# Kernel optimization log

Measured on AMD Instinct MI355X. Metric: run time of the kernel, lower is better.

## Reference

```python
import jax, jax.numpy as jnp
import numpy as np

N_NODES = 1048576
N_SEG = 16384
NODES_PER_SEG = N_NODES // N_SEG
D = 128
EPS = 1e-5


def setup_inputs() -> dict:
    key = jax.random.key(0)
    ks = jax.random.split(key, 8)
    feat = jax.random.normal(ks[0], (N_NODES, D), dtype=jnp.float32)
    position_weight = jax.random.uniform(ks[1], (N_NODES,), dtype=jnp.float32)
    # equal-size segments (sessions): contiguous, sorted segment ids
    segment_ids = jnp.repeat(jnp.arange(N_SEG, dtype=jnp.int32), NODES_PER_SEG)
    # last node of each segment
    last_nodes = jnp.arange(N_SEG, dtype=jnp.int32) * NODES_PER_SEG + (NODES_PER_SEG - 1)
    # parameters
    gamma = jnp.ones((D,), dtype=jnp.float32)
    beta = jnp.zeros((D,), dtype=jnp.float32)
    s = 1.0 / np.sqrt(D)
    W_u = jax.random.uniform(ks[2], (D, D), dtype=jnp.float32, minval=-s, maxval=s)
    W_i = jax.random.uniform(ks[3], (D, D), dtype=jnp.float32, minval=-s, maxval=s)
    b_i = jax.random.uniform(ks[4], (D,), dtype=jnp.float32, minval=-s, maxval=s)
    w_e = jax.random.uniform(ks[5], (D,), dtype=jnp.float32, minval=-s, maxval=s)
    return {
        "feat": feat, "position_weight": position_weight,
        "last_nodes": last_nodes, "segment_ids": segment_ids,
        "gamma": gamma, "beta": beta, "W_u": W_u, "W_i": W_i,
        "b_i": b_i, "w_e": w_e, "num_segments": N_SEG,
    }


def reference(feat, position_weight, last_nodes, segment_ids, gamma, beta,
              W_u, W_i, b_i, w_e, num_segments):
    # BatchNorm1d (training-mode batch statistics)
    mean = feat.mean(axis=0)
    var = jnp.mean((feat - mean) ** 2, axis=0)
    f = (feat - mean) * (gamma / jnp.sqrt(var + EPS)) + beta  # [N, D]

    feat_u = f @ W_u.T                                         # [N, H]
    feat_last = f[last_nodes] @ W_i.T + b_i                    # [B, H]
    # broadcast_nodes: gather per-graph vector back to its nodes
    e = jax.nn.sigmoid(feat_u + feat_last[segment_ids]) @ w_e  # [N]

    # segment softmax over nodes of each graph
    m = jax.ops.segment_max(e, segment_ids, num_segments=num_segments)
    ex = jnp.exp(e - m[segment_ids])
    denom = jax.ops.segment_sum(ex, segment_ids, num_segments=num_segments)
    alpha = ex / denom[segment_ids]                            # [N]

    rst = jax.ops.segment_sum(f * alpha[:, None], segment_ids,
                              num_segments=num_segments)       # [B, D]
    position_rst = jax.ops.segment_sum(f * position_weight[:, None], segment_ids,
                                       num_segments=num_segments)  # [B, D]
    return rst, position_rst
```

## Files before the change

### kernel.cpp

```cpp
#include <hip/hip_runtime.h>

#define N_NODES 1048576
#define N_SEG   16384
#define NPS     64
#define D       128
#define EPS     1e-5f

typedef float f4 __attribute__((ext_vector_type(4)));
typedef float f32x4 __attribute__((ext_vector_type(4)));
typedef __bf16 bf16x8 __attribute__((ext_vector_type(8)));

__global__ __launch_bounds__(256) void k_stats(const float* __restrict__ feat,
                                               float* __restrict__ part) {
    int t = threadIdx.x;
    long gid = (long)blockIdx.x * 256 + t;
    const f4* f4p = (const f4*)feat;
    f4 s = {0.f,0.f,0.f,0.f}, q = {0.f,0.f,0.f,0.f};
#pragma unroll 8
    for (int k = 0; k < 64; ++k) {
        f4 v = f4p[gid + (long)k * 524288];
        s += v;
        q += v * v;
    }
    __shared__ f4 red[2][8][32];
    red[0][t >> 5][t & 31] = s;
    red[1][t >> 5][t & 31] = q;
    __syncthreads();
    int stat = t >> 7, c = t & 127;
    const float* base = (const float*)&red[stat][0][0];
    float acc = 0.f;
#pragma unroll
    for (int r = 0; r < 8; ++r) acc += base[r * 128 + c];
    part[(stat * 128 + c) * 2048 + blockIdx.x] = acc;
}

__global__ __launch_bounds__(256) void k_scale(const float* __restrict__ part,
                                               const float* __restrict__ gamma,
                                               const float* __restrict__ beta,
                                               float* __restrict__ scl,
                                               float* __restrict__ shf) {
    int t = threadIdx.x, c = blockIdx.x;
    float s1 = 0.f, s2 = 0.f;
#pragma unroll
    for (int j = 0; j < 8; ++j) {
        s1 += part[c * 2048 + t + 256 * j];
        s2 += part[(128 + c) * 2048 + t + 256 * j];
    }
    __shared__ float rs[256], rq[256];
    rs[t] = s1; rq[t] = s2;
    __syncthreads();
    for (int off = 128; off > 0; off >>= 1) {
        if (t < off) { rs[t] += rs[t + off]; rq[t] += rq[t + off]; }
        __syncthreads();
    }
    if (t == 0) {
        float mean = rs[0] / (float)N_NODES;
        float var  = rq[0] / (float)N_NODES - mean * mean;
        float sc   = gamma[c] * rsqrtf(var + EPS);
        scl[c] = sc;
        shf[c] = beta[c] - mean * sc;
    }
}

__device__ inline unsigned pk2(float x, float y) {
    unsigned a = __builtin_bit_cast(unsigned, x);
    unsigned b = __builtin_bit_cast(unsigned, y);
    a = (a + 0x7fffu + ((a >> 16) & 1u)) >> 16;
    b = (b + 0x7fffu + ((b >> 16) & 1u)) & 0xffff0000u;
    return a | b;
}
__device__ inline bf16x8 lds8(const unsigned short* p, int row, int kb) {
    int addr = (row * 256 + kb) ^ ((row & 7) << 4);
    return *(const bf16x8*)((const char*)p + addr);
}

__global__ __launch_bounds__(256)
void k_main(const float* __restrict__ feat,
            const float* __restrict__ pw,
            const float* __restrict__ Wu,
            const float* __restrict__ Wi,
            const float* __restrict__ bi,
            const float* __restrict__ we,
            const float* __restrict__ scl,
            const float* __restrict__ shf,
            float* __restrict__ out) {
    __shared__ __align__(16) unsigned short sW[128 * 128];
    __shared__ __align__(16) unsigned short abuf[64 * 128];
    __shared__ float flp_s[8][128];
    __shared__ float pw_s[512];
    __shared__ float epart[4][64];
    __shared__ float wpR[4][128];
    __shared__ float wpP[4][128];

    int t = threadIdx.x;
    int lane = t & 63, w = t >> 6;
    int l15 = lane & 15, g4 = lane >> 4;
    int c0 = 4 * (t & 31);
    f4 vscl = *(const f4*)(scl + c0);
    f4 vshf = *(const f4*)(shf + c0);
    int h_a = l15 + 32 * w;
    int h_b = h_a + 16;
    int seg0 = blockIdx.x * 8;

    pw_s[t] = pw[seg0 * NPS + t];
    pw_s[t + 256] = pw[seg0 * NPS + t + 256];
    {
        int r = t >> 5;
        long row = (long)(seg0 + r) * NPS + (NPS - 1);
        f4 v = *(const f4*)(feat + row * 128 + c0);
        v = v * vscl + vshf;
        int addr = (r * 256 + 8 * (t & 31)) ^ ((r & 7) << 4);
        *(uint2*)((char*)abuf + addr) = make_uint2(pk2(v.x, v.y), pk2(v.z, v.w));
        int r2 = r + 8;
        int addr2 = (r2 * 256 + 8 * (t & 31)) ^ ((r2 & 7) << 4);
        *(uint2*)((char*)abuf + addr2) = make_uint2(0u, 0u);
    }
    {
        const f4* W4 = (const f4*)Wi;
#pragma unroll
        for (int k = 0; k < 16; ++k) {
            int g = t + 256 * k, h = g >> 5, cq = g & 31;
            f4 v = W4[g];
            int addr = (h * 256 + cq * 8) ^ ((h & 7) << 4);
            *(uint2*)((char*)sW + addr) = make_uint2(pk2(v.x, v.y), pk2(v.z, v.w));
        }
    }
    __syncthreads();
    {
        f32x4 a2[2];
        a2[0] = (f32x4){0.f,0.f,0.f,0.f};
        a2[1] = (f32x4){0.f,0.f,0.f,0.f};
#pragma unroll
        for (int kk = 0; kk < 4; ++kk) {
            int kb = kk * 64 + g4 * 16;
            bf16x8 a = lds8(abuf, l15, kb);
            a2[0] = __builtin_amdgcn_mfma_f32_16x16x32_bf16(a, lds8(sW, h_a, kb), a2[0], 0, 0, 0);
            a2[1] = __builtin_amdgcn_mfma_f32_16x16x32_bf16(a, lds8(sW, h_b, kb), a2[1], 0, 0, 0);
        }
        float bia = bi[h_a], bib = bi[h_b];
#pragma unroll
        for (int r = 0; r < 4; ++r) {
            int si = 4 * g4 + r;
            if (si < 8) {
                flp_s[si][h_a] = a2[0][r] + bia;
                flp_s[si][h_b] = a2[1][r] + bib;
            }
        }
    }
    __syncthreads();
    {
        const f4* W4 = (const f4*)Wu;
#pragma unroll
        for (int k = 0; k < 16; ++k) {
            int g = t + 256 * k, h = g >> 5, cq = g & 31;
            f4 v = W4[g];
            int addr = (h * 256 + cq * 8) ^ ((h & 7) << 4);
            *(uint2*)((char*)sW + addr) = make_uint2(pk2(v.x, v.y), pk2(v.z, v.w));
        }
    }
    float we0 = we[h_a], we1 = we[h_b];
    __syncthreads();

    for (int it = 0; it < 8; ++it) {
        int seg = seg0 + it;
        {
            const f4* src = (const f4*)(feat + (long)seg * NPS * D);
#pragma unroll
            for (int k = 0; k < 8; ++k) {
                f4 v = src[t + 256 * k] * vscl + vshf;
                int n = (t >> 5) + 8 * k;
                int addr = (n * 256 + 8 * (t & 31)) ^ ((n & 7) << 4);
                *(uint2*)((char*)abuf + addr) = make_uint2(pk2(v.x, v.y), pk2(v.z, v.w));
            }
        }
        __syncthreads();

        float fl0 = flp_s[it][h_a];
        float fl1 = flp_s[it][h_b];
        float eacc[4][4];
#pragma unroll
        for (int nf = 0; nf < 4; ++nf)
#pragma unroll
            for (int r = 0; r < 4; ++r) eacc[nf][r] = 0.f;
#pragma unroll
        for (int hfp = 0; hfp < 2; ++hfp) {
            int h = hfp ? h_b : h_a;
            float flh = hfp ? fl1 : fl0;
            float weh = hfp ? we1 : we0;
            f32x4 acc[4];
#pragma unroll
            for (int nf = 0; nf < 4; ++nf) acc[nf] = (f32x4){0.f,0.f,0.f,0.f};
#pragma unroll
            for (int kk = 0; kk < 4; ++kk) {
                int kb = kk * 64 + g4 * 16;
                bf16x8 b = lds8(sW, h, kb);
#pragma unroll
                for (int nf = 0; nf < 4; ++nf) {
                    bf16x8 a = lds8(abuf, l15 + 16 * nf, kb);
                    acc[nf] = __builtin_amdgcn_mfma_f32_16x16x32_bf16(a, b, acc[nf], 0, 0, 0);
                }
            }
#pragma unroll
            for (int nf = 0; nf < 4; ++nf)
#pragma unroll
                for (int r = 0; r < 4; ++r) {
                    float x = acc[nf][r] + flh;
                    eacc[nf][r] += weh * __frcp_rn(1.f + __expf(-x));
                }
        }
#pragma unroll
        for (int nf = 0; nf < 4; ++nf) {
#pragma unroll
            for (int r = 0; r < 4; ++r) {
                float p = eacc[nf][r];
                p += __shfl_xor(p, 1);
                p += __shfl_xor(p, 2);
                p += __shfl_xor(p, 4);
                p += __shfl_xor(p, 8);
                if (l15 == 0) epart[w][16 * nf + 4 * g4 + r] = p;
            }
        }
        __syncthreads();

        float e = epart[0][lane] + epart[1][lane] + epart[2][lane] + epart[3][lane];
        float m = e;
#pragma unroll
        for (int off = 32; off > 0; off >>= 1) m = fmaxf(m, __shfl_xor(m, off));
        float ex = __expf(e - m);
        float sd = ex;
#pragma unroll
        for (int off = 32; off > 0; off >>= 1) sd += __shfl_xor(sd, off);
        float al = ex / sd;

        f4 racc = {0.f,0.f,0.f,0.f}, pacc = {0.f,0.f,0.f,0.f};
#pragma unroll
        for (int k = 0; k < 8; ++k) {
            int n = (t >> 5) + 8 * k;
            int addr = (n * 256 + 8 * (t & 31)) ^ ((n & 7) << 4);
            uint2 u = *(const uint2*)((const char*)abuf + addr);
            f4 fv;
            fv.x = __builtin_bit_cast(float, u.x << 16);
            fv.y = __builtin_bit_cast(float, u.x & 0xffff0000u);
            fv.z = __builtin_bit_cast(float, u.y << 16);
            fv.w = __builtin_bit_cast(float, u.y & 0xffff0000u);
            float av = __shfl(al, n);
            float pv = pw_s[it * NPS + n];
            racc += av * fv;
            pacc += pv * fv;
        }
#pragma unroll
        for (int c = 0; c < 4; ++c) {
            racc[c] += __shfl_xor(racc[c], 32);
            pacc[c] += __shfl_xor(pacc[c], 32);
        }
        if (lane < 32) {
            *(f4*)&wpR[w][4 * lane] = racc;
            *(f4*)&wpP[w][4 * lane] = pacc;
        }
        __syncthreads();

        if (t < 128) {
            out[(long)seg * 128 + t] = wpR[0][t] + wpR[1][t] + wpR[2][t] + wpR[3][t];
        } else {
            int c = t - 128;
            out[(long)N_SEG * 128 + (long)seg * 128 + c] =
                wpP[0][c] + wpP[1][c] + wpP[2][c] + wpP[3][c];
        }
    }
}

extern "C" void kernel_launch(void* const* d_in, const int* in_sizes, int n_in,
                              void* d_out, int out_size, void* d_ws, size_t ws_size,
                              hipStream_t stream) {
    const float* feat       = (const float*)d_in[0];
    const float* pw         = (const float*)d_in[1];
    const float* gamma      = (const float*)d_in[4];
    const float* beta       = (const float*)d_in[5];
    const float* Wu         = (const float*)d_in[6];
    const float* Wi         = (const float*)d_in[7];
    const float* bi         = (const float*)d_in[8];
    const float* we         = (const float*)d_in[9];
    float* out = (float*)d_out;

    float* ws   = (float*)d_ws;
    float* part = ws;
    float* wscl = ws + 524288;
    float* wshf = ws + 524288 + 128;

    k_stats<<<dim3(2048), dim3(256), 0, stream>>>(feat, part);
    k_scale<<<dim3(128),  dim3(256), 0, stream>>>(part, gamma, beta, wscl, wshf);
    k_main <<<dim3(2048), dim3(256), 0, stream>>>(feat, pw, Wu, Wi, bi, we, wscl, wshf, out);
}
```

Before: 358.5 us.

## Assign whole segments per wavefront, loading MFMA operands directly from global memory

```diff
diff --git a/kernel.cpp b/kernel.cpp
--- a/kernel.cpp
+++ b/kernel.cpp
@@ -85,35 +85,31 @@
             const float* __restrict__ shf,
             float* __restrict__ out) {
     __shared__ __align__(16) unsigned short sW[128 * 128];
-    __shared__ __align__(16) unsigned short abuf[64 * 128];
+    __shared__ __align__(16) unsigned short sA8[16 * 128];
     __shared__ float flp_s[8][128];
-    __shared__ float pw_s[512];
-    __shared__ float epart[4][64];
-    __shared__ float wpR[4][128];
-    __shared__ float wpP[4][128];
+    __shared__ float scl_s[128], shf_s[128], we_s[128];
+    __shared__ float alpha_w[4][64];
+    __shared__ float pw_w[4][64];
 
     int t = threadIdx.x;
     int lane = t & 63, w = t >> 6;
     int l15 = lane & 15, g4 = lane >> 4;
     int c0 = 4 * (t & 31);
-    f4 vscl = *(const f4*)(scl + c0);
-    f4 vshf = *(const f4*)(shf + c0);
-    int h_a = l15 + 32 * w;
-    int h_b = h_a + 16;
     int seg0 = blockIdx.x * 8;
 
-    pw_s[t] = pw[seg0 * NPS + t];
-    pw_s[t + 256] = pw[seg0 * NPS + t + 256];
+    if (t < 128) { scl_s[t] = scl[t]; shf_s[t] = shf[t]; we_s[t] = we[t]; }
     {
         int r = t >> 5;
         long row = (long)(seg0 + r) * NPS + (NPS - 1);
         f4 v = *(const f4*)(feat + row * 128 + c0);
-        v = v * vscl + vshf;
+        f4 vs = *(const f4*)(scl + c0);
+        f4 vh = *(const f4*)(shf + c0);
+        v = v * vs + vh;
         int addr = (r * 256 + 8 * (t & 31)) ^ ((r & 7) << 4);
-        *(uint2*)((char*)abuf + addr) = make_uint2(pk2(v.x, v.y), pk2(v.z, v.w));
+        *(uint2*)((char*)sA8 + addr) = make_uint2(pk2(v.x, v.y), pk2(v.z, v.w));
         int r2 = r + 8;
         int addr2 = (r2 * 256 + 8 * (t & 31)) ^ ((r2 & 7) << 4);
-        *(uint2*)((char*)abuf + addr2) = make_uint2(0u, 0u);
+        *(uint2*)((char*)sA8 + addr2) = make_uint2(0u, 0u);
     }
     {
         const f4* W4 = (const f4*)Wi;
@@ -127,13 +123,14 @@
     }
     __syncthreads();
     {
+        int h_a = l15 + 32 * w, h_b = h_a + 16;
         f32x4 a2[2];
         a2[0] = (f32x4){0.f,0.f,0.f,0.f};
         a2[1] = (f32x4){0.f,0.f,0.f,0.f};
 #pragma unroll
         for (int kk = 0; kk < 4; ++kk) {
             int kb = kk * 64 + g4 * 16;
-            bf16x8 a = lds8(abuf, l15, kb);
+            bf16x8 a = lds8(sA8, l15, kb);
             a2[0] = __builtin_amdgcn_mfma_f32_16x16x32_bf16(a, lds8(sW, h_a, kb), a2[0], 0, 0, 0);
             a2[1] = __builtin_amdgcn_mfma_f32_16x16x32_bf16(a, lds8(sW, h_b, kb), a2[1], 0, 0, 0);
         }
@@ -158,113 +155,95 @@
             *(uint2*)((char*)sW + addr) = make_uint2(pk2(v.x, v.y), pk2(v.z, v.w));
         }
     }
-    float we0 = we[h_a], we1 = we[h_b];
-    __syncthreads();
-
-    for (int it = 0; it < 8; ++it) {
-        int seg = seg0 + it;
-        {
-            const f4* src = (const f4*)(feat + (long)seg * NPS * D);
-#pragma unroll
-            for (int k = 0; k < 8; ++k) {
-                f4 v = src[t + 256 * k] * vscl + vshf;
-                int n = (t >> 5) + 8 * k;
-                int addr = (n * 256 + 8 * (t & 31)) ^ ((n & 7) << 4);
-                *(uint2*)((char*)abuf + addr) = make_uint2(pk2(v.x, v.y), pk2(v.z, v.w));
+    __syncthreads();
+
+    for (int s = 0; s < 2; ++s) {
+        int sl = 2 * w + s, seg = seg0 + sl;
+        const float* fb = feat + (long)seg * NPS * D;
+
+        pw_w[w][lane] = pw[seg * NPS + lane];
+
+        float e_c[4];
+#pragma unroll
+        for (int c = 0; c < 4; ++c) {
+            bf16x8 af[4];
+#pragma unroll
+            for (int kk = 0; kk < 4; ++kk) {
+                int d0 = kk * 32 + g4 * 8;
+                const float* p = fb + (16 * c + l15) * 128 + d0;
+                f4 u = *(const f4*)p, v = *(const f4*)(p + 4);
+                f4 s1 = *(const f4*)&scl_s[d0], s2 = *(const f4*)&scl_s[d0 + 4];
+                f4 h1 = *(const f4*)&shf_s[d0], h2 = *(const f4*)&shf_s[d0 + 4];
+                u = u * s1 + h1;
+                v = v * s2 + h2;
+                unsigned r0 = pk2(u.x, u.y), r1 = pk2(u.z, u.w);
+                unsigned r2 = pk2(v.x, v.y), r3 = pk2(v.z, v.w);
+                uint4 rr = make_uint4(r0, r1, r2, r3);
+                af[kk] = __builtin_bit_cast(bf16x8, rr);
             }
-        }
-        __syncthreads();
-
-        float fl0 = flp_s[it][h_a];
-        float fl1 = flp_s[it][h_b];
-        float eacc[4][4];
-#pragma unroll
-        for (int nf = 0; nf < 4; ++nf)
-#pragma unroll
-            for (int r = 0; r < 4; ++r) eacc[nf][r] = 0.f;
-#pragma unroll
-        for (int hfp = 0; hfp < 2; ++hfp) {
-            int h = hfp ? h_b : h_a;
-            float flh = hfp ? fl1 : fl0;
-            float weh = hfp ? we1 : we0;
-            f32x4 acc[4];
-#pragma unroll
-            for (int nf = 0; nf < 4; ++nf) acc[nf] = (f32x4){0.f,0.f,0.f,0.f};
-#pragma unroll
-            for (int kk = 0; kk < 4; ++kk) {
-                int kb = kk * 64 + g4 * 16;
-                bf16x8 b = lds8(sW, h, kb);
-#pragma unroll
-                for (int nf = 0; nf < 4; ++nf) {
-                    bf16x8 a = lds8(abuf, l15 + 16 * nf, kb);
-                    acc[nf] = __builtin_amdgcn_mfma_f32_16x16x32_bf16(a, b, acc[nf], 0, 0, 0);
+            float eacc = 0.f;
+#pragma unroll
+            for (int hf = 0; hf < 8; ++hf) {
+                f32x4 acc = (f32x4){0.f,0.f,0.f,0.f};
+#pragma unroll
+                for (int kk = 0; kk < 4; ++kk) {
+                    bf16x8 wuf = lds8(sW, 16 * hf + l15, kk * 64 + g4 * 16);
+                    acc = __builtin_amdgcn_mfma_f32_16x16x32_bf16(wuf, af[kk], acc, 0, 0, 0);
+                }
+                f4 flp4 = *(const f4*)&flp_s[sl][16 * hf + 4 * g4];
+                f4 we4  = *(const f4*)&we_s[16 * hf + 4 * g4];
+#pragma unroll
+                for (int r = 0; r < 4; ++r) {
+                    float x = acc[r] + flp4[r];
+                    eacc += we4[r] * __frcp_rn(1.f + __expf(-x));
                 }
             }
-#pragma unroll
-            for (int nf = 0; nf < 4; ++nf)
-#pragma unroll
-                for (int r = 0; r < 4; ++r) {
-                    float x = acc[nf][r] + flh;
-                    eacc[nf][r] += weh * __frcp_rn(1.f + __expf(-x));
-                }
-        }
-#pragma unroll
-        for (int nf = 0; nf < 4; ++nf) {
-#pragma unroll
-            for (int r = 0; r < 4; ++r) {
-                float p = eacc[nf][r];
-                p += __shfl_xor(p, 1);
-                p += __shfl_xor(p, 2);
-                p += __shfl_xor(p, 4);
-                p += __shfl_xor(p, 8);
-                if (l15 == 0) epart[w][16 * nf + 4 * g4 + r] = p;
-            }
-        }
-        __syncthreads();
-
-        float e = epart[0][lane] + epart[1][lane] + epart[2][lane] + epart[3][lane];
-        float m = e;
-#pragma unroll
-        for (int off = 32; off > 0; off >>= 1) m = fmaxf(m, __shfl_xor(m, off));
-        float ex = __expf(e - m);
-        float sd = ex;
-#pragma unroll
-        for (int off = 32; off > 0; off >>= 1) sd += __shfl_xor(sd, off);
-        float al = ex / sd;
-
+            eacc += __shfl_xor(eacc, 16);
+            eacc += __shfl_xor(eacc, 32);
+            e_c[c] = eacc;
+        }
+
+        float m = fmaxf(fmaxf(e_c[0], e_c[1]), fmaxf(e_c[2], e_c[3]));
+#pragma unroll
+        for (int off = 8; off > 0; off >>= 1) m = fmaxf(m, __shfl_xor(m, off));
+        float a0 = __expf(e_c[0] - m), a1 = __expf(e_c[1] - m);
+        float a2 = __expf(e_c[2] - m), a3 = __expf(e_c[3] - m);
+        float sd = a0 + a1 + a2 + a3;
+#pragma unroll
+        for (int off = 8; off > 0; off >>= 1) sd += __shfl_xor(sd, off);
+        float inv = 1.f / sd;
+        if (g4 == 0) {
+            alpha_w[w][l15]      = a0 * inv;
+            alpha_w[w][16 + l15] = a1 * inv;
+            alpha_w[w][32 + l15] = a2 * inv;
+            alpha_w[w][48 + l15] = a3 * inv;
+        }
+        float spw = pw_w[w][lane];
+#pragma unroll
+        for (int off = 32; off > 0; off >>= 1) spw += __shfl_xor(spw, off);
+
+        int q = lane >> 5, cc = lane & 31;
         f4 racc = {0.f,0.f,0.f,0.f}, pacc = {0.f,0.f,0.f,0.f};
-#pragma unroll
-        for (int k = 0; k < 8; ++k) {
-            int n = (t >> 5) + 8 * k;
-            int addr = (n * 256 + 8 * (t & 31)) ^ ((n & 7) << 4);
-            uint2 u = *(const uint2*)((const char*)abuf + addr);
-            f4 fv;
-            fv.x = __builtin_bit_cast(float, u.x << 16);
-            fv.y = __builtin_bit_cast(float, u.x & 0xffff0000u);
-            fv.z = __builtin_bit_cast(float, u.y << 16);
-            fv.w = __builtin_bit_cast(float, u.y & 0xffff0000u);
-            float av = __shfl(al, n);
-            float pv = pw_s[it * NPS + n];
-            racc += av * fv;
-            pacc += pv * fv;
-        }
-#pragma unroll
-        for (int c = 0; c < 4; ++c) {
-            racc[c] += __shfl_xor(racc[c], 32);
-            pacc[c] += __shfl_xor(pacc[c], 32);
+#pragma unroll 4
+        for (int k = 0; k < 32; ++k) {
+            int n = q + 2 * k;
+            f4 v = *(const f4*)(fb + n * 128 + cc * 4);
+            float al = alpha_w[w][n];
+            float pv = pw_w[w][n];
+            racc += al * v;
+            pacc += pv * v;
+        }
+#pragma unroll
+        for (int j = 0; j < 4; ++j) {
+            racc[j] += __shfl_xor(racc[j], 32);
+            pacc[j] += __shfl_xor(pacc[j], 32);
         }
         if (lane < 32) {
-            *(f4*)&wpR[w][4 * lane] = racc;
-            *(f4*)&wpP[w][4 * lane] = pacc;
-        }
-        __syncthreads();
-
-        if (t < 128) {
-            out[(long)seg * 128 + t] = wpR[0][t] + wpR[1][t] + wpR[2][t] + wpR[3][t];
-        } else {
-            int c = t - 128;
-            out[(long)N_SEG * 128 + (long)seg * 128 + c] =
-                wpP[0][c] + wpP[1][c] + wpP[2][c] + wpP[3][c];
+            f4 sc4 = *(const f4*)&scl_s[4 * cc];
+            f4 sh4 = *(const f4*)&shf_s[4 * cc];
+            *(f4*)(out + (long)seg * 128 + 4 * cc) = sc4 * racc + sh4;
+            *(f4*)(out + (long)N_SEG * 128 + (long)seg * 128 + 4 * cc) =
+                sc4 * pacc + sh4 * spw;
         }
     }
 }
```

Result: slower. 517.8 us (+44.4%).

## Process two segments per iteration and prefetch next pair's features into registers

Applied to the files above, without the earlier changes.

```diff
diff --git a/kernel.cpp b/kernel.cpp
--- a/kernel.cpp
+++ b/kernel.cpp
@@ -73,6 +73,12 @@
     int addr = (row * 256 + kb) ^ ((row & 7) << 4);
     return *(const bf16x8*)((const char*)p + addr);
 }
+__device__ inline void barx() {
+    __builtin_amdgcn_sched_barrier(0);
+    asm volatile("s_waitcnt lgkmcnt(0)");
+    __builtin_amdgcn_s_barrier();
+    __builtin_amdgcn_sched_barrier(0);
+}
 
 __global__ __launch_bounds__(256)
 void k_main(const float* __restrict__ feat,
@@ -85,12 +91,11 @@
             const float* __restrict__ shf,
             float* __restrict__ out) {
     __shared__ __align__(16) unsigned short sW[128 * 128];
-    __shared__ __align__(16) unsigned short abuf[64 * 128];
+    __shared__ __align__(16) unsigned short abuf[128 * 128];
     __shared__ float flp_s[8][128];
-    __shared__ float pw_s[512];
-    __shared__ float epart[4][64];
-    __shared__ float wpR[4][128];
-    __shared__ float wpP[4][128];
+    __shared__ float epart[4][128];
+    __shared__ float wpR[2][4][128];
+    __shared__ float wpP[2][4][128];
 
     int t = threadIdx.x;
     int lane = t & 63, w = t >> 6;
@@ -98,12 +103,17 @@
     int c0 = 4 * (t & 31);
     f4 vscl = *(const f4*)(scl + c0);
     f4 vshf = *(const f4*)(shf + c0);
-    int h_a = l15 + 32 * w;
-    int h_b = h_a + 16;
+    int h_a = l15 + 32 * w, h_b = h_a + 16;
     int seg0 = blockIdx.x * 8;
 
-    pw_s[t] = pw[seg0 * NPS + t];
-    pw_s[t + 256] = pw[seg0 * NPS + t + 256];
+    f4 fn[16];
+    {
+        const f4* src = (const f4*)(feat + (long)seg0 * NPS * D);
+#pragma unroll
+        for (int k = 0; k < 16; ++k) fn[k] = src[t + 256 * k];
+    }
+    __builtin_amdgcn_sched_barrier(0);
+
     {
         int r = t >> 5;
         long row = (long)(seg0 + r) * NPS + (NPS - 1);
@@ -125,7 +135,7 @@
             *(uint2*)((char*)sW + addr) = make_uint2(pk2(v.x, v.y), pk2(v.z, v.w));
         }
     }
-    __syncthreads();
+    barx();
     {
         f32x4 a2[2];
         a2[0] = (f32x4){0.f,0.f,0.f,0.f};
@@ -147,7 +157,7 @@
             }
         }
     }
-    __syncthreads();
+    barx();
     {
         const f4* W4 = (const f4*)Wu;
 #pragma unroll
@@ -159,82 +169,93 @@
         }
     }
     float we0 = we[h_a], we1 = we[h_b];
-    __syncthreads();
-
-    for (int it = 0; it < 8; ++it) {
-        int seg = seg0 + it;
-        {
-            const f4* src = (const f4*)(feat + (long)seg * NPS * D);
-#pragma unroll
-            for (int k = 0; k < 8; ++k) {
-                f4 v = src[t + 256 * k] * vscl + vshf;
-                int n = (t >> 5) + 8 * k;
-                int addr = (n * 256 + 8 * (t & 31)) ^ ((n & 7) << 4);
-                *(uint2*)((char*)abuf + addr) = make_uint2(pk2(v.x, v.y), pk2(v.z, v.w));
-            }
-        }
-        __syncthreads();
-
-        float fl0 = flp_s[it][h_a];
-        float fl1 = flp_s[it][h_b];
-        float eacc[4][4];
-#pragma unroll
-        for (int nf = 0; nf < 4; ++nf)
-#pragma unroll
-            for (int r = 0; r < 4; ++r) eacc[nf][r] = 0.f;
-#pragma unroll
-        for (int hfp = 0; hfp < 2; ++hfp) {
-            int h = hfp ? h_b : h_a;
-            float flh = hfp ? fl1 : fl0;
-            float weh = hfp ? we1 : we0;
-            f32x4 acc[4];
-#pragma unroll
-            for (int nf = 0; nf < 4; ++nf) acc[nf] = (f32x4){0.f,0.f,0.f,0.f};
-#pragma unroll
-            for (int kk = 0; kk < 4; ++kk) {
-                int kb = kk * 64 + g4 * 16;
-                bf16x8 b = lds8(sW, h, kb);
-#pragma unroll
-                for (int nf = 0; nf < 4; ++nf) {
-                    bf16x8 a = lds8(abuf, l15 + 16 * nf, kb);
-                    acc[nf] = __builtin_amdgcn_mfma_f32_16x16x32_bf16(a, b, acc[nf], 0, 0, 0);
-                }
-            }
-#pragma unroll
-            for (int nf = 0; nf < 4; ++nf)
-#pragma unroll
-                for (int r = 0; r < 4; ++r) {
-                    float x = acc[nf][r] + flh;
-                    eacc[nf][r] += weh * __frcp_rn(1.f + __expf(-x));
-                }
-        }
-#pragma unroll
-        for (int nf = 0; nf < 4; ++nf) {
-#pragma unroll
-            for (int r = 0; r < 4; ++r) {
-                float p = eacc[nf][r];
-                p += __shfl_xor(p, 1);
-                p += __shfl_xor(p, 2);
-                p += __shfl_xor(p, 4);
-                p += __shfl_xor(p, 8);
-                if (l15 == 0) epart[w][16 * nf + 4 * g4 + r] = p;
-            }
-        }
-        __syncthreads();
-
-        float e = epart[0][lane] + epart[1][lane] + epart[2][lane] + epart[3][lane];
-        float m = e;
-#pragma unroll
-        for (int off = 32; off > 0; off >>= 1) m = fmaxf(m, __shfl_xor(m, off));
-        float ex = __expf(e - m);
-        float sd = ex;
-#pragma unroll
-        for (int off = 32; off > 0; off >>= 1) sd += __shfl_xor(sd, off);
-        float al = ex / sd;
-
-        f4 racc = {0.f,0.f,0.f,0.f}, pacc = {0.f,0.f,0.f,0.f};
-#pragma unroll
-        for (int k = 0; k < 8; ++k) {
+    barx();
+
+#define GATE_SEG(SL, RB)                                                          \
+    do {                                                                          \
+        float fl0_ = flp_s[(SL)][h_a];                                            \
+        float fl1_ = flp_s[(SL)][h_b];                                            \
+        f32x4 acc[4][2];                                                          \
+        _Pragma("unroll")                                                         \
+        for (int nf = 0; nf < 4; ++nf) {                                          \
+            acc[nf][0] = (f32x4){0.f,0.f,0.f,0.f};                                \
+            acc[nf][1] = (f32x4){0.f,0.f,0.f,0.f};                                \
+        }                                                                         \
+        _Pragma("unroll")                                                         \
+        for (int kk = 0; kk < 4; ++kk) {                                          \
+            int kb = kk * 64 + g4 * 16;                                           \
+            bf16x8 a[4];                                                          \
+            _Pragma("unroll")                                                     \
+            for (int nf = 0; nf < 4; ++nf) a[nf] = lds8(abuf, (RB) + l15 + 16 * nf, kb); \
+            _Pragma("unroll")                                                     \
+            for (int nf = 0; nf < 4; ++nf) {                                      \
+                acc[nf][0] = __builtin_amdgcn_mfma_f32_16x16x32_bf16(a[nf], lds8(sW, h_a, kb), acc[nf][0], 0, 0, 0); \
+                acc[nf][1] = __builtin_amdgcn_mfma_f32_16x16x32_bf16(a[nf], lds8(sW, h_b, kb), acc[nf][1], 0, 0, 0); \
+            }                                                                     \
+        }                                                                         \
+        _Pragma("unroll")                                                         \
+        for (int nf = 0; nf < 4; ++nf) {                                          \
+            _Pragma("unroll")                                                     \
+            for (int r = 0; r < 4; ++r) {                                         \
+                float x0 = acc[nf][0][r] + fl0_;                                  \
+                float x1 = acc[nf][1][r] + fl1_;                                  \
+                float p = we0 * __frcp_rn(1.f + __expf(-x0))                      \
+                        + we1 * __frcp_rn(1.f + __expf(-x1));                     \
+                p += __shfl_xor(p, 1);                                            \
+                p += __shfl_xor(p, 2);                                            \
+                p += __shfl_xor(p, 4);                                            \
+                p += __shfl_xor(p, 8);                                            \
+                if (l15 == 0) epart[w][(RB) + 16 * nf + 4 * g4 + r] = p;          \
+            }                                                                     \
+        }                                                                         \
+    } while (0)
+
+    for (int it = 0; it < 4; ++it) {
+        int sA = 2 * it, sB = 2 * it + 1;
+        int segA = seg0 + sA, segB = seg0 + sB;
+
+#pragma unroll
+        for (int k = 0; k < 16; ++k) {
+            f4 v = fn[k] * vscl + vshf;
+            int n = (t >> 5) + 8 * k;
+            int addr = (n * 256 + 8 * (t & 31)) ^ ((n & 7) << 4);
+            *(uint2*)((char*)abuf + addr) = make_uint2(pk2(v.x, v.y), pk2(v.z, v.w));
+        }
+        barx();
+        if (it < 3) {
+            const f4* src = (const f4*)(feat + (long)(seg0 + 2 * it + 2) * NPS * D);
+#pragma unroll
+            for (int k = 0; k < 16; ++k) fn[k] = src[t + 256 * k];
+        }
+        __builtin_amdgcn_sched_barrier(0);
+
+        GATE_SEG(sA, 0);
+        GATE_SEG(sB, 64);
+        barx();
+
+        float eA = epart[0][lane] + epart[1][lane] + epart[2][lane] + epart[3][lane];
+        float eB = epart[0][64 + lane] + epart[1][64 + lane]
+                 + epart[2][64 + lane] + epart[3][64 + lane];
+        float mA = eA, mB = eB;
+#pragma unroll
+        for (int off = 32; off > 0; off >>= 1) {
+            mA = fmaxf(mA, __shfl_xor(mA, off));
+            mB = fmaxf(mB, __shfl_xor(mB, off));
+        }
+        float exA = __expf(eA - mA), exB = __expf(eB - mB);
+        float sdA = exA, sdB = exB;
+#pragma unroll
+        for (int off = 32; off > 0; off >>= 1) {
+            sdA += __shfl_xor(sdA, off);
+            sdB += __shfl_xor(sdB, off);
+        }
+        float alA = exA / sdA;
+        float alB = exB / sdB;
+
+        f4 rA = {0.f,0.f,0.f,0.f}, pA = {0.f,0.f,0.f,0.f};
+        f4 rB = {0.f,0.f,0.f,0.f}, pB = {0.f,0.f,0.f,0.f};
+#pragma unroll
+        for (int k = 0; k < 16; ++k) {
             int n = (t >> 5) + 8 * k;
             int addr = (n * 256 + 8 * (t & 31)) ^ ((n & 7) << 4);
             uint2 u = *(const uint2*)((const char*)abuf + addr);
@@ -243,30 +264,48 @@
             fv.y = __builtin_bit_cast(float, u.x & 0xffff0000u);
             fv.z = __builtin_bit_cast(float, u.y << 16);
             fv.w = __builtin_bit_cast(float, u.y & 0xffff0000u);
-            float av = __shfl(al, n);
-            float pv = pw_s[it * NPS + n];
-            racc += av * fv;
-            pacc += pv * fv;
+            if (k < 8) {
+                float av = __shfl(alA, n);
+                float pv = pw[segA * NPS + n];
+                rA += av * fv;
+                pA += pv * fv;
+            } else {
+                int nb = n - 64;
+                float av = __shfl(alB, nb);
+                float pv = pw[segB * NPS + nb];
+                rB += av * fv;
+                pB += pv * fv;
+            }
         }
 #pragma unroll
         for (int c = 0; c < 4; ++c) {
-            racc[c] += __shfl_xor(racc[c], 32);
-            pacc[c] += __shfl_xor(pacc[c], 32);
+            rA[c] += __shfl_xor(rA[c], 32);
+            pA[c] += __shfl_xor(pA[c], 32);
+            rB[c] += __shfl_xor(rB[c], 32);
+            pB[c] += __shfl_xor(pB[c], 32);
         }
         if (lane < 32) {
-            *(f4*)&wpR[w][4 * lane] = racc;
-            *(f4*)&wpP[w][4 * lane] = pacc;
-        }
-        __syncthreads();
+            *(f4*)&wpR[0][w][4 * lane] = rA;
+            *(f4*)&wpP[0][w][4 * lane] = pA;
+            *(f4*)&wpR[1][w][4 * lane] = rB;
+            *(f4*)&wpP[1][w][4 * lane] = pB;
+        }
+        barx();
 
         if (t < 128) {
-            out[(long)seg * 128 + t] = wpR[0][t] + wpR[1][t] + wpR[2][t] + wpR[3][t];
+            out[(long)segA * 128 + t] =
+                wpR[0][0][t] + wpR[0][1][t] + wpR[0][2][t] + wpR[0][3][t];
+            out[(long)segB * 128 + t] =
+                wpR[1][0][t] + wpR[1][1][t] + wpR[1][2][t] + wpR[1][3][t];
         } else {
             int c = t - 128;
-            out[(long)N_SEG * 128 + (long)seg * 128 + c] =
-                wpP[0][c] + wpP[1][c] + wpP[2][c] + wpP[3][c];
-        }
-    }
+            out[(long)N_SEG * 128 + (long)segA * 128 + c] =
+                wpP[0][0][c] + wpP[0][1][c] + wpP[0][2][c] + wpP[0][3][c];
+            out[(long)N_SEG * 128 + (long)segB * 128 + c] =
+                wpP[1][0][c] + wpP[1][1][c] + wpP[1][2][c] + wpP[1][3][c];
+        }
+    }
+#undef GATE_SEG
 }
 
 extern "C" void kernel_launch(void* const* d_in, const int* in_sizes, int n_in,
```

After: 532.3 us. 1.48x slower.
